# Kernel tuning notes

Measured on AMD Instinct MI355X. Metric: run time of the kernel, lower is better.

## Reference

```python
import jax, jax.numpy as jnp
import numpy as np

FG_THR = 0.7
BG_THR = 0.3
NUM_PER_IMAGE = 256
NUM_POS_MAX = int(NUM_PER_IMAGE * 0.5)  # positive_ratio = 0.5
BBOX_W = (1.0, 1.0, 1.0, 1.0)
BETA = 1.0 / 9.0


def _permute(t, C):
    # N x (A*C) x H x W -> N x (H*W*A) x C, matching RPNLoss.permute
    N, _, H, W = t.shape
    t = t.reshape(N, -1, C, H, W)
    t = jnp.transpose(t, (0, 3, 4, 1, 2))
    return t.reshape(N, -1, C)


def _iou(a, b):
    # a: [N,4], b: [M,4] -> [N,M] (with +1 box convention, as in source)
    x_tl = jnp.maximum(a[:, None, 0], b[None, :, 0])
    y_tl = jnp.maximum(a[:, None, 1], b[None, :, 1])
    x_rb = jnp.minimum(a[:, None, 2], b[None, :, 2])
    y_rb = jnp.minimum(a[:, None, 3], b[None, :, 3])
    inter = jnp.clip(x_rb - x_tl + 1.0, 0.0) * jnp.clip(y_rb - y_tl + 1.0, 0.0)
    area1 = (a[:, 2] - a[:, 0] + 1.0) * (a[:, 3] - a[:, 1] + 1.0)
    area2 = (b[:, 2] - b[:, 0] + 1.0) * (b[:, 3] - b[:, 1] + 1.0)
    return inter / (area1[:, None] + area2[None, :] - inter)


def _encode(anchors, targets):
    ws = anchors[:, 2] - anchors[:, 0] + 1.0
    hs = anchors[:, 3] - anchors[:, 1] + 1.0
    x_ctr = anchors[:, 0] + 0.5 * ws
    y_ctr = anchors[:, 1] + 0.5 * hs
    t_ws = targets[:, 2] - targets[:, 0] + 1.0
    t_hs = targets[:, 3] - targets[:, 1] + 1.0
    t_x = targets[:, 0] + 0.5 * t_ws
    t_y = targets[:, 1] + 0.5 * t_hs
    wx, wy, ww, wh = BBOX_W
    tx = wx * (t_x - x_ctr) / ws
    ty = wy * (t_y - y_ctr) / hs
    tw = ww * jnp.log(t_ws / ws)
    th = wh * jnp.log(t_hs / hs)
    return jnp.stack([tx, ty, tw, th], axis=1)


def _bce_logits(l, t):
    return jnp.maximum(l, 0.0) - l * t + jnp.log1p(jnp.exp(-jnp.abs(l)))


def _per_image(anchor, logit, breg, size, target, key):
    N = anchor.shape[0]
    ious = _iou(anchor, target)  # [N, M]
    vals = ious.max(axis=1)
    ori = jnp.argmax(ious, axis=1).astype(jnp.int32)
    inds = jnp.where(vals < BG_THR, -1, ori)
    inds = jnp.where((vals >= BG_THR) & (vals < FG_THR), -2, inds)
    # low-quality matches: anchors achieving the per-target max IoU keep their argmax
    col_max = ious.max(axis=0)
    restore = (ious == col_max[None, :]).any(axis=1)
    inds = jnp.where(restore, ori, inds)
    # filter_anchors: keep anchors fully inside the image (size = (h, w))
    inside = (anchor[:, 0] >= 0) & (anchor[:, 1] >= 0) & \
             (anchor[:, 2] <= size[1] - 1.0) & (anchor[:, 3] <= size[0] - 1.0)
    inds = jnp.where(inside, inds, -2)

    pos = inds >= 0
    neg = inds == -1
    # random sampling via random priorities + fixed-size top_k with validity masks
    r = jax.random.uniform(key, (N,))
    pos_vals, pos_idx = jax.lax.top_k(jnp.where(pos, r, -1.0), NUM_POS_MAX)
    valid_pos = pos_vals >= 0.0
    num_pos = valid_pos.sum()
    neg_vals, neg_idx = jax.lax.top_k(jnp.where(neg, r, -1.0), NUM_PER_IMAGE)
    valid_neg = (neg_vals >= 0.0) & (jnp.arange(NUM_PER_IMAGE) < (NUM_PER_IMAGE - num_pos))

    # classification loss terms (BCE with logits); pos target 1, neg target 0
    vp = valid_pos.astype(logit.dtype)
    vn = valid_neg.astype(logit.dtype)
    cls_sum = jnp.sum(_bce_logits(logit[pos_idx], 1.0) * vp) + \
              jnp.sum(_bce_logits(logit[neg_idx], 0.0) * vn)
    count = num_pos + valid_neg.sum()

    m = jnp.clip(inds[pos_idx], 0, None)
    offsets = _encode(anchor[pos_idx], target[m])
    diff = jnp.abs(breg[pos_idx] - offsets)
    sl1 = jnp.where(diff < BETA, 0.5 * diff * diff / BETA, diff - 0.5 * BETA)
    reg_sum = jnp.sum(sl1 * vp[:, None])
    return cls_sum, count, reg_sum


def reference(anchors, logits, bbox_regs, sizes, targets):
    B = anchors.shape[0]
    log = _permute(logits, 1)[..., 0]      # [B, H*W*A]
    breg = _permute(bbox_regs, 4)          # [B, H*W*A, 4]
    keys = jax.random.split(jax.random.key(42), B)
    cls_s, cnt, reg_s = jax.vmap(_per_image)(anchors, log, breg, sizes, targets, keys)
    total = jnp.sum(cnt).astype(anchors.dtype)
    cls_loss = jnp.sum(cls_s) / total
    reg_loss = jnp.sum(reg_s) / total
    return jnp.stack([cls_loss, reg_loss])


def setup_inputs() -> dict:
    key = jax.random.key(0)
    ks = jax.random.split(key, 10)
    B, A, H, W, M = 4, 3, 168, 256, 32
    N = H * W * A
    IMG_H, IMG_W = 800.0, 1333.0
    x1 = jax.random.uniform(ks[0], (B, N)) * 1200.0
    y1 = jax.random.uniform(ks[1], (B, N)) * 700.0
    aw = jax.random.uniform(ks[2], (B, N)) * 300.0 + 16.0
    ah = jax.random.uniform(ks[3], (B, N)) * 300.0 + 16.0
    anchors = jnp.stack([x1, y1, x1 + aw, y1 + ah], axis=-1)  # some out of image -> filtered
    tx1 = jax.random.uniform(ks[4], (B, M)) * 1000.0
    ty1 = jax.random.uniform(ks[5], (B, M)) * 500.0
    tw = jax.random.uniform(ks[6], (B, M)) * 250.0 + 30.0
    th = jax.random.uniform(ks[7], (B, M)) * 200.0 + 30.0
    targets = jnp.stack([tx1, ty1, jnp.minimum(tx1 + tw, IMG_W - 1.0),
                         jnp.minimum(ty1 + th, IMG_H - 1.0)], axis=-1)
    logits = jax.random.normal(ks[8], (B, A, H, W), dtype=jnp.float32)
    bbox_regs = jax.random.normal(ks[9], (B, 4 * A, H, W), dtype=jnp.float32) * 0.1
    sizes = jnp.tile(jnp.array([IMG_H, IMG_W], dtype=jnp.float32), (B, 1))
    return {"anchors": anchors, "logits": logits, "bbox_regs": bbox_regs,
            "sizes": sizes, "targets": targets}
```

## Files before the change

### kernel.cpp

```cpp
#include <hip/hip_runtime.h>
#include <stdint.h>

#define Bn 4
#define An 3
#define Hn 168
#define Wn 256
#define Mn 32
#define HWn (Hn*Wn)
#define Nn (HWn*An)
#define POS_CAP 8192
#define BND_CAP 2048
#define NPERIM 256
#define NPOSMAX 128
#define FG_THR 0.7f
#define BG_THR 0.3f
#define BETA (1.0f/9.0f)

#define OFF_KEYS   0
#define OFF_COLMAX 8
#define OFF_POSCNT 136
#define OFF_BNDCNT 140
#define OFF_BOUND  144
#define OFF_NEED   148
#define OFF_COUNT  152
#define OFF_CLS    153
#define OFF_REG    154
#define OFF_DONE   155
#define ZERO_BEG   8
#define ZERO_END   160
#define OFF_PACK   4256
#define OFF_PLIST  520352
#define OFF_BLIST  585888
#define OFF_PHIST  602272

__device__ __forceinline__ uint32_t rotl32(uint32_t v, int n) { return (v << n) | (v >> (32 - n)); }

__device__ __forceinline__ void tf2x32(uint32_t k0, uint32_t k1, uint32_t x0, uint32_t x1,
                                       uint32_t& o0, uint32_t& o1) {
    uint32_t k2 = k0 ^ k1 ^ 0x1BD11BDAu;
    x0 += k0; x1 += k1;
    x0 += x1; x1 = rotl32(x1, 13); x1 ^= x0;
    x0 += x1; x1 = rotl32(x1, 15); x1 ^= x0;
    x0 += x1; x1 = rotl32(x1, 26); x1 ^= x0;
    x0 += x1; x1 = rotl32(x1, 6);  x1 ^= x0;
    x0 += k1; x1 += k2 + 1u;
    x0 += x1; x1 = rotl32(x1, 17); x1 ^= x0;
    x0 += x1; x1 = rotl32(x1, 29); x1 ^= x0;
    x0 += x1; x1 = rotl32(x1, 16); x1 ^= x0;
    x0 += x1; x1 = rotl32(x1, 24); x1 ^= x0;
    x0 += k2; x1 += k0 + 2u;
    x0 += x1; x1 = rotl32(x1, 13); x1 ^= x0;
    x0 += x1; x1 = rotl32(x1, 15); x1 ^= x0;
    x0 += x1; x1 = rotl32(x1, 26); x1 ^= x0;
    x0 += x1; x1 = rotl32(x1, 6);  x1 ^= x0;
    x0 += k0; x1 += k1 + 3u;
    x0 += x1; x1 = rotl32(x1, 17); x1 ^= x0;
    x0 += x1; x1 = rotl32(x1, 29); x1 ^= x0;
    x0 += x1; x1 = rotl32(x1, 16); x1 ^= x0;
    x0 += x1; x1 = rotl32(x1, 24); x1 ^= x0;
    x0 += k1; x1 += k2 + 4u;
    x0 += x1; x1 = rotl32(x1, 13); x1 ^= x0;
    x0 += x1; x1 = rotl32(x1, 15); x1 ^= x0;
    x0 += x1; x1 = rotl32(x1, 26); x1 ^= x0;
    x0 += x1; x1 = rotl32(x1, 6);  x1 ^= x0;
    x0 += k2; x1 += k0 + 5u;
    o0 = x0; o1 = x1;
}

__device__ __forceinline__ uint32_t rng_m23(uint32_t k0, uint32_t k1, uint32_t i) {
    uint32_t o0, o1;
    tf2x32(k0, k1, 0u, i, o0, o1);
    return (o0 ^ o1) >> 9;
}

__device__ __forceinline__ float iou_one(float a0, float a1, float a2, float a3,
                                         float t0, float t1, float t2, float t3) {
    float xtl = fmaxf(a0, t0), ytl = fmaxf(a1, t1);
    float xrb = fminf(a2, t2), yrb = fminf(a3, t3);
    float iw = fmaxf(xrb - xtl + 1.0f, 0.0f);
    float ih = fmaxf(yrb - ytl + 1.0f, 0.0f);
    float inter = iw * ih;
    float area1 = (a2 - a0 + 1.0f) * (a3 - a1 + 1.0f);
    float area2 = (t2 - t0 + 1.0f) * (t3 - t1 + 1.0f);
    return inter * __builtin_amdgcn_rcpf(area1 + area2 - inter);
}

__global__ void k0_init(uint32_t* __restrict__ ws) {
    int t = blockIdx.x * blockDim.x + threadIdx.x;
    for (int j = ZERO_BEG + t; j < ZERO_END; j += gridDim.x * blockDim.x) ws[j] = 0u;
    if (t == 0) {
        for (int b = 0; b < Bn; ++b) {
            uint32_t o0, o1;
            tf2x32(0u, 42u, 0u, (uint32_t)b, o0, o1);
            ws[OFF_KEYS + 2*b] = o0; ws[OFF_KEYS + 2*b + 1] = o1;
        }
    }
}

#define K1_APT 4
#define K1_BLOCKS 126
#define K1_STRIDE (K1_BLOCKS * 256)
__global__ void __launch_bounds__(256) k1_colmax(const float* __restrict__ anchors,
                                                 const float* __restrict__ targets,
                                                 uint32_t* __restrict__ ws) {
    int b = blockIdx.y;
    __shared__ float part[4][Mn];
    int base = blockIdx.x * 256 + threadIdx.x;
    float4 a[K1_APT];
    #pragma unroll
    for (int k = 0; k < K1_APT; ++k)
        a[k] = ((const float4*)anchors)[b * Nn + base + k * K1_STRIDE];
    float cm[Mn];
    #pragma unroll 4
    for (int t = 0; t < Mn; ++t) {
        float4 tv = ((const float4*)targets)[b * Mn + t];
        float m0 = 0.0f;
        #pragma unroll
        for (int k = 0; k < K1_APT; ++k)
            m0 = fmaxf(m0, iou_one(a[k].x, a[k].y, a[k].z, a[k].w, tv.x, tv.y, tv.z, tv.w));
        cm[t] = m0;
    }
    #pragma unroll
    for (int t = 0; t < Mn; ++t) {
        #pragma unroll
        for (int o = 32; o > 0; o >>= 1) cm[t] = fmaxf(cm[t], __shfl_xor(cm[t], o, 64));
    }
    int wid = threadIdx.x >> 6, lane = threadIdx.x & 63;
    if (lane == 0) {
        #pragma unroll
        for (int t = 0; t < Mn; ++t) part[wid][t] = cm[t];
    }
    __syncthreads();
    if (threadIdx.x < Mn) {
        float v = fmaxf(fmaxf(part[0][threadIdx.x], part[1][threadIdx.x]),
                        fmaxf(part[2][threadIdx.x], part[3][threadIdx.x]));
        atomicMax(&ws[OFF_COLMAX + b * Mn + threadIdx.x], __float_as_uint(v));
    }
}

#define K2_APT 4
#define K2_BLOCKS 126
#define K2_STRIDE (K2_BLOCKS * 256)
__global__ void __launch_bounds__(256) k2_cat(const float* __restrict__ anchors,
                                              const float* __restrict__ targets,
                                              const float* __restrict__ sizes,
                                              uint32_t* __restrict__ ws) {
    int b = blockIdx.y;
    __shared__ uint32_t lh[1024];
    #pragma unroll
    for (int j = 0; j < 4; ++j) lh[threadIdx.x + 256 * j] = 0u;
    __syncthreads();
    int base = blockIdx.x * 256 + threadIdx.x;
    float4 av[K2_APT];
    #pragma unroll
    for (int k = 0; k < K2_APT; ++k)
        av[k] = ((const float4*)anchors)[b * Nn + base + k * K2_STRIDE];
    float rowmax[K2_APT]; int ori[K2_APT]; bool restore[K2_APT];
    #pragma unroll
    for (int k = 0; k < K2_APT; ++k) { rowmax[k] = -1.0f; ori[k] = 0; restore[k] = false; }
    #pragma unroll 4
    for (int t = 0; t < Mn; ++t) {
        float4 tv = ((const float4*)targets)[b * Mn + t];
        float cmf = __uint_as_float(ws[OFF_COLMAX + b * Mn + t]);
        #pragma unroll
        for (int k = 0; k < K2_APT; ++k) {
            float iou = iou_one(av[k].x, av[k].y, av[k].z, av[k].w, tv.x, tv.y, tv.z, tv.w);
            if (iou > rowmax[k]) { rowmax[k] = iou; ori[k] = t; }
            restore[k] = restore[k] || (iou == cmf);
        }
    }
    float sh = sizes[b * 2 + 0], sw = sizes[b * 2 + 1];
    uint32_t key0 = ws[OFF_KEYS + 2 * b], key1 = ws[OFF_KEYS + 2 * b + 1];
    #pragma unroll
    for (int k = 0; k < K2_APT; ++k) {
        int i = base + k * K2_STRIDE;
        bool inside = (av[k].x >= 0.0f) && (av[k].y >= 0.0f) &&
                      (av[k].z <= sw - 1.0f) && (av[k].w <= sh - 1.0f);
        uint32_t cat = 0;
        if (inside) {
            if (restore[k] || rowmax[k] >= FG_THR) cat = 2;
            else if (rowmax[k] < BG_THR) cat = 1;
        }
        uint32_t m = rng_m23(key0, key1, (uint32_t)i);
        ws[OFF_PACK + b * Nn + i] = m | (cat << 24);
        if (cat == 2u) {
            uint32_t p = atomicAdd(&ws[OFF_POSCNT + b], 1u);
            if (p < POS_CAP) {
                ws[OFF_PLIST + ((uint32_t)b * POS_CAP + p) * 2 + 0] = m;
                ws[OFF_PLIST + ((uint32_t)b * POS_CAP + p) * 2 + 1] = (uint32_t)i | ((uint32_t)ori[k] << 17);
            }
        } else if (cat == 1u) {
            atomicAdd(&lh[m >> 13], 1u);
        }
    }
    __syncthreads();
    uint32_t* slice = ws + OFF_PHIST + ((size_t)b * K2_BLOCKS + blockIdx.x) * 1024;
    #pragma unroll
    for (int j = 0; j < 4; ++j) {
        int idx = threadIdx.x + 256 * j;
        slice[idx] = lh[idx];
    }
}

__global__ void __launch_bounds__(256) k25_bound(uint32_t* __restrict__ ws) {
    int b = blockIdx.x;
    int t = threadIdx.x;
    __shared__ uint32_t csum[256];
    uint4 h = make_uint4(0, 0, 0, 0);
    const uint32_t* ph = ws + OFF_PHIST + (size_t)b * K2_BLOCKS * 1024;
    for (int s = 0; s < K2_BLOCKS; ++s) {
        uint4 v = ((const uint4*)(ph + (size_t)s * 1024))[t];
        h.x += v.x; h.y += v.y; h.z += v.z; h.w += v.w;
    }
    uint32_t sum = h.x + h.y + h.z + h.w;
    csum[t] = sum;
    __syncthreads();
    for (int off = 1; off < 256; off <<= 1) {
        uint32_t mine = csum[t];
        uint32_t add = (t + off < 256) ? csum[t + off] : 0u;
        __syncthreads();
        csum[t] = mine + add;
        __syncthreads();
    }
    uint32_t pc = ws[OFF_POSCNT + b];
    int num_pos = (pc < (uint32_t)NPOSMAX) ? (int)pc : NPOSMAX;
    int k_neg = NPERIM - num_pos;
    uint32_t total = csum[0];
    if ((int)total < k_neg) {
        if (t == 0) {
            ws[OFF_BOUND + b] = 0xFFFFFFFFu;
            ws[OFF_NEED + b] = 0u;
            atomicAdd(&ws[OFF_COUNT], (uint32_t)(num_pos + (int)total));
        }
        return;
    }
    uint32_t incl = csum[t];
    uint32_t next = (t < 255) ? csum[t + 1] : 0u;
    if ((int)incl >= k_neg && (int)next < k_neg) {
        int cum = (int)next;
        uint32_t hv[4] = { h.x, h.y, h.z, h.w };
        int boundary = -1, needed = 0;
        #pragma unroll
        for (int j = 3; j >= 0; --j) {
            int c = (int)hv[j];
            if (cum + c >= k_neg) { boundary = 4 * t + j; needed = k_neg - cum; break; }
            cum += c;
        }
        ws[OFF_BOUND + b] = (uint32_t)boundary;
        ws[OFF_NEED + b] = (uint32_t)needed;
        atomicAdd(&ws[OFF_COUNT], (uint32_t)(num_pos + k_neg));
    }
}

__global__ void __launch_bounds__(256) k3_neg(const float* __restrict__ logits,
                                              uint32_t* __restrict__ ws) {
    int b = blockIdx.y;
    int i = blockIdx.x * 256 + threadIdx.x;
    int bd = (int)(int32_t)ws[OFF_BOUND + b];
    uint32_t p = ws[OFF_PACK + b * Nn + i];
    uint32_t cat = p >> 24;
    float local = 0.0f;
    if (cat == 1u) {
        uint32_t m = p & 0x7FFFFFu;
        int bk = (int)(m >> 13);
        if (bk > bd) {
            int a = i % An, hw = i / An;
            float l = logits[(b * An + a) * HWn + hw];
            local = fmaxf(l, 0.0f) + log1pf(expf(-fabsf(l)));
        } else if (bk == bd) {
            uint32_t q = atomicAdd(&ws[OFF_BNDCNT + b], 1u);
            if (q < BND_CAP) {
                ws[OFF_BLIST + ((uint32_t)b * BND_CAP + q) * 2 + 0] = m;
                ws[OFF_BLIST + ((uint32_t)b * BND_CAP + q) * 2 + 1] = (uint32_t)i;
            }
        }
    }
    __shared__ float red[256];
    red[threadIdx.x] = local;
    __syncthreads();
    for (int s = 128; s > 0; s >>= 1) {
        if ((int)threadIdx.x < s) red[threadIdx.x] += red[threadIdx.x + s];
        __syncthreads();
    }
    if (threadIdx.x == 0 && red[0] != 0.0f) atomicAdd((float*)&ws[OFF_CLS], red[0]);
}

__device__ __forceinline__ bool sel_less(uint2 a, uint2 b) {
    return (a.x > b.x) || (a.x == b.x && a.y < b.y);
}

__device__ void bitonic_sort_shared(uint2* buf, int n) {
    for (int k = 2; k <= n; k <<= 1) {
        for (int j = k >> 1; j > 0; j >>= 1) {
            for (int t = (int)threadIdx.x; t < n; t += 256) {
                int ixj = t ^ j;
                if (ixj > t) {
                    uint2 x = buf[t], y = buf[ixj];
                    bool up = ((t & k) == 0);
                    bool sw = up ? sel_less(y, x) : sel_less(x, y);
                    if (sw) { buf[t] = y; buf[ixj] = x; }
                }
            }
            __syncthreads();
        }
    }
}

__global__ void __launch_bounds__(256) k4_final(const float* __restrict__ anchors,
                                                const float* __restrict__ targets,
                                                const float* __restrict__ logits,
                                                const float* __restrict__ bregs,
                                                uint32_t* __restrict__ ws,
                                                float* __restrict__ out) {
    int b = blockIdx.x;
    __shared__ uint2 buf[BND_CAP];
    __shared__ float red[256];
    float cls = 0.0f, reg = 0.0f;

    uint32_t pcu = ws[OFF_POSCNT + b];
    int pc = (pcu < (uint32_t)POS_CAP) ? (int)pcu : POS_CAP;
    const uint32_t* plist = ws + OFF_PLIST + (size_t)b * POS_CAP * 2;
    int psel = (pc < NPOSMAX) ? pc : NPOSMAX;
    bool use_buf = false;
    if (pc > NPOSMAX) {
        int n = (pc < BND_CAP) ? pc : BND_CAP;
        for (int j = (int)threadIdx.x; j < n; j += 256) buf[j] = make_uint2(plist[2*j], plist[2*j+1]);
        int npad = 1; while (npad < n) npad <<= 1;
        for (int j = (int)threadIdx.x; j < npad; j += 256) if (j >= n) buf[j] = make_uint2(0u, 0xFFFFFFFFu);
        __syncthreads();
        bitonic_sort_shared(buf, npad);
        use_buf = true;
        psel = (NPOSMAX < n) ? NPOSMAX : n;
    }
    for (int j = (int)threadIdx.x; j < psel; j += 256) {
        uint32_t packed = use_buf ? buf[j].y : plist[2*j+1];
        int i = (int)(packed & 0x1FFFFu);
        int ori = (int)(packed >> 17);
        int a = i % An, hw = i / An;
        float l = logits[(b * An + a) * HWn + hw];
        cls += fmaxf(l, 0.0f) - l + log1pf(expf(-fabsf(l)));
        float4 av = ((const float4*)anchors)[b * Nn + i];
        float4 tv = ((const float4*)targets)[b * Mn + ori];
        float aws = av.z - av.x + 1.0f, ahs = av.w - av.y + 1.0f;
        float axc = av.x + 0.5f * aws, ayc = av.y + 0.5f * ahs;
        float tws = tv.z - tv.x + 1.0f, ths = tv.w - tv.y + 1.0f;
        float txc = tv.x + 0.5f * tws, tyc = tv.y + 0.5f * ths;
        float off0 = (txc - axc) / aws;
        float off1 = (tyc - ayc) / ahs;
        float off2 = logf(tws / aws);
        float off3 = logf(ths / ahs);
        float br0 = bregs[(b * 12 + a * 4 + 0) * HWn + hw];
        float br1 = bregs[(b * 12 + a * 4 + 1) * HWn + hw];
        float br2 = bregs[(b * 12 + a * 4 + 2) * HWn + hw];
        float br3 = bregs[(b * 12 + a * 4 + 3) * HWn + hw];
        float d;
        d = fabsf(br0 - off0); reg += (d < BETA) ? 0.5f * d * d / BETA : d - 0.5f * BETA;
        d = fabsf(br1 - off1); reg += (d < BETA) ? 0.5f * d * d / BETA : d - 0.5f * BETA;
        d = fabsf(br2 - off2); reg += (d < BETA) ? 0.5f * d * d / BETA : d - 0.5f * BETA;
        d = fabsf(br3 - off3); reg += (d < BETA) ? 0.5f * d * d / BETA : d - 0.5f * BETA;
    }
    __syncthreads();

    int need = (int)ws[OFF_NEED + b];
    if (need > 0) {
        uint32_t nbu = ws[OFF_BNDCNT + b];
        int nb = (nbu < (uint32_t)BND_CAP) ? (int)nbu : BND_CAP;
        const uint32_t* blist = ws + OFF_BLIST + (size_t)b * BND_CAP * 2;
        for (int j = (int)threadIdx.x; j < nb; j += 256) buf[j] = make_uint2(blist[2*j], blist[2*j+1]);
        int npad = 1; while (npad < nb) npad <<= 1;
        for (int j = (int)threadIdx.x; j < npad; j += 256) if (j >= nb) buf[j] = make_uint2(0u, 0xFFFFFFFFu);
        __syncthreads();
        bitonic_sort_shared(buf, npad);
        int sel = (need < nb) ? need : nb;
        for (int j = (int)threadIdx.x; j < sel; j += 256) {
            int i = (int)buf[j].y;
            int a = i % An, hw = i / An;
            float l = logits[(b * An + a) * HWn + hw];
            cls += fmaxf(l, 0.0f) + log1pf(expf(-fabsf(l)));
        }
    }

    red[threadIdx.x] = cls;
    __syncthreads();
    for (int s = 128; s > 0; s >>= 1) {
        if ((int)threadIdx.x < s) red[threadIdx.x] += red[threadIdx.x + s];
        __syncthreads();
    }
    if (threadIdx.x == 0 && red[0] != 0.0f) atomicAdd((float*)&ws[OFF_CLS], red[0]);
    __syncthreads();
    red[threadIdx.x] = reg;
    __syncthreads();
    for (int s = 128; s > 0; s >>= 1) {
        if ((int)threadIdx.x < s) red[threadIdx.x] += red[threadIdx.x + s];
        __syncthreads();
    }
    if (threadIdx.x == 0) {
        if (red[0] != 0.0f) atomicAdd((float*)&ws[OFF_REG], red[0]);
        __threadfence();
        uint32_t old = atomicAdd(&ws[OFF_DONE], 1u);
        if (old == Bn - 1) {
            float cls_tot = __uint_as_float(atomicAdd(&ws[OFF_CLS], 0u));
            float reg_tot = __uint_as_float(atomicAdd(&ws[OFF_REG], 0u));
            float cnt = (float)atomicAdd(&ws[OFF_COUNT], 0u);
            out[0] = cls_tot / cnt;
            out[1] = reg_tot / cnt;
        }
    }
}

extern "C" void kernel_launch(void* const* d_in, const int* in_sizes, int n_in,
                              void* d_out, int out_size, void* d_ws, size_t ws_size,
                              hipStream_t stream) {
    const float* anchors = (const float*)d_in[0];
    const float* logits  = (const float*)d_in[1];
    const float* bregs   = (const float*)d_in[2];
    const float* sizes   = (const float*)d_in[3];
    const float* targets = (const float*)d_in[4];
    float* out = (float*)d_out;
    uint32_t* ws = (uint32_t*)d_ws;

    k0_init<<<dim3(64), dim3(256), 0, stream>>>(ws);
    k1_colmax<<<dim3(K1_BLOCKS, Bn), dim3(256), 0, stream>>>(anchors, targets, ws);
    k2_cat<<<dim3(K2_BLOCKS, Bn), dim3(256), 0, stream>>>(anchors, targets, sizes, ws);
    k25_bound<<<dim3(Bn), dim3(256), 0, stream>>>(ws);
    k3_neg<<<dim3(Nn / 256, Bn), dim3(256), 0, stream>>>(logits, ws);
    k4_final<<<dim3(Bn), dim3(256), 0, stream>>>(anchors, targets, logits, bregs, ws, out);
}
```

Baseline: 161.7 us.

## Compact negatives into a list, drop init kernel, wave-aggregate atomics

Removes the separate init kernel by having one k1 block zero the counters and derive the keys, and replaces the global atomicMax column max with per-block partials that k2 reduces itself. k2 now writes a compacted negative list using wave-level ballot atomics instead of a full packed array, and positive-list appends also use ballot-aggregated atomics. k3 then walks only the negative list with a grid-stride loop instead of scanning every anchor. This cuts one launch and much of the global traffic and contention, but k2 must first reduce the partial column maxes, and the negative list is written with no capacity bound.

```diff
diff --git a/kernel.cpp b/kernel.cpp
--- a/kernel.cpp
+++ b/kernel.cpp
@@ -10,28 +10,33 @@
 #define Nn (HWn*An)
 #define POS_CAP 8192
 #define BND_CAP 2048
+#define NEG_CAP 131072
 #define NPERIM 256
 #define NPOSMAX 128
 #define FG_THR 0.7f
 #define BG_THR 0.3f
 #define BETA (1.0f/9.0f)
 
-#define OFF_KEYS   0
-#define OFF_COLMAX 8
-#define OFF_POSCNT 136
-#define OFF_BNDCNT 140
-#define OFF_BOUND  144
-#define OFF_NEED   148
-#define OFF_COUNT  152
-#define OFF_CLS    153
-#define OFF_REG    154
-#define OFF_DONE   155
-#define ZERO_BEG   8
-#define ZERO_END   160
-#define OFF_PACK   4256
-#define OFF_PLIST  520352
-#define OFF_BLIST  585888
-#define OFF_PHIST  602272
+#define NBLK 126
+#define APT 4
+#define STRIDE (NBLK * 256)
+
+#define OFF_POSCNT 0
+#define OFF_NEGCNT 4
+#define OFF_BNDCNT 8
+#define OFF_BOUND  12
+#define OFF_NEED   16
+#define OFF_COUNT  20
+#define OFF_CLS    21
+#define OFF_REG    22
+#define OFF_DONE   23
+#define OFF_KEYS   24
+#define OFF_PCM    32
+#define OFF_PHIST  16160
+#define OFF_FHIST  532256
+#define OFF_PLIST  536352
+#define OFF_BLIST  601888
+#define OFF_NLIST  618272
 
 __device__ __forceinline__ uint32_t rotl32(uint32_t v, int n) { return (v << n) | (v >> (32 - n)); }
 
@@ -85,38 +90,33 @@
     return inter * __builtin_amdgcn_rcpf(area1 + area2 - inter);
 }
 
-__global__ void k0_init(uint32_t* __restrict__ ws) {
-    int t = blockIdx.x * blockDim.x + threadIdx.x;
-    for (int j = ZERO_BEG + t; j < ZERO_END; j += gridDim.x * blockDim.x) ws[j] = 0u;
-    if (t == 0) {
-        for (int b = 0; b < Bn; ++b) {
-            uint32_t o0, o1;
-            tf2x32(0u, 42u, 0u, (uint32_t)b, o0, o1);
-            ws[OFF_KEYS + 2*b] = o0; ws[OFF_KEYS + 2*b + 1] = o1;
-        }
-    }
-}
-
-#define K1_APT 4
-#define K1_BLOCKS 126
-#define K1_STRIDE (K1_BLOCKS * 256)
 __global__ void __launch_bounds__(256) k1_colmax(const float* __restrict__ anchors,
                                                  const float* __restrict__ targets,
                                                  uint32_t* __restrict__ ws) {
-    int b = blockIdx.y;
+    int b = blockIdx.y, j = blockIdx.x, tid = threadIdx.x;
+    if (b == 0 && j == 0) {
+        if (tid < 24) ws[tid] = 0u;
+        if (tid == 0) {
+            for (int bb = 0; bb < Bn; ++bb) {
+                uint32_t o0, o1;
+                tf2x32(0u, 42u, 0u, (uint32_t)bb, o0, o1);
+                ws[OFF_KEYS + 2*bb] = o0; ws[OFF_KEYS + 2*bb + 1] = o1;
+            }
+        }
+    }
     __shared__ float part[4][Mn];
-    int base = blockIdx.x * 256 + threadIdx.x;
-    float4 a[K1_APT];
-    #pragma unroll
-    for (int k = 0; k < K1_APT; ++k)
-        a[k] = ((const float4*)anchors)[b * Nn + base + k * K1_STRIDE];
+    int base = j * 256 + tid;
+    float4 a[APT];
+    #pragma unroll
+    for (int k = 0; k < APT; ++k)
+        a[k] = ((const float4*)anchors)[b * Nn + base + k * STRIDE];
     float cm[Mn];
     #pragma unroll 4
     for (int t = 0; t < Mn; ++t) {
         float4 tv = ((const float4*)targets)[b * Mn + t];
         float m0 = 0.0f;
         #pragma unroll
-        for (int k = 0; k < K1_APT; ++k)
+        for (int k = 0; k < APT; ++k)
             m0 = fmaxf(m0, iou_one(a[k].x, a[k].y, a[k].z, a[k].w, tv.x, tv.y, tv.z, tv.w));
         cm[t] = m0;
     }
@@ -125,55 +125,70 @@
         #pragma unroll
         for (int o = 32; o > 0; o >>= 1) cm[t] = fmaxf(cm[t], __shfl_xor(cm[t], o, 64));
     }
-    int wid = threadIdx.x >> 6, lane = threadIdx.x & 63;
+    int wid = tid >> 6, lane = tid & 63;
     if (lane == 0) {
         #pragma unroll
         for (int t = 0; t < Mn; ++t) part[wid][t] = cm[t];
     }
     __syncthreads();
-    if (threadIdx.x < Mn) {
-        float v = fmaxf(fmaxf(part[0][threadIdx.x], part[1][threadIdx.x]),
-                        fmaxf(part[2][threadIdx.x], part[3][threadIdx.x]));
-        atomicMax(&ws[OFF_COLMAX + b * Mn + threadIdx.x], __float_as_uint(v));
-    }
-}
-
-#define K2_APT 4
-#define K2_BLOCKS 126
-#define K2_STRIDE (K2_BLOCKS * 256)
+    if (tid < Mn) {
+        float v = fmaxf(fmaxf(part[0][tid], part[1][tid]),
+                        fmaxf(part[2][tid], part[3][tid]));
+        ws[OFF_PCM + ((size_t)b * NBLK + j) * Mn + tid] = __float_as_uint(v);
+    }
+}
+
 __global__ void __launch_bounds__(256) k2_cat(const float* __restrict__ anchors,
                                               const float* __restrict__ targets,
                                               const float* __restrict__ sizes,
                                               uint32_t* __restrict__ ws) {
-    int b = blockIdx.y;
+    int b = blockIdx.y, j = blockIdx.x, tid = threadIdx.x;
+    __shared__ float cmf[Mn];
+    __shared__ float redf[256];
     __shared__ uint32_t lh[1024];
-    #pragma unroll
-    for (int j = 0; j < 4; ++j) lh[threadIdx.x + 256 * j] = 0u;
-    __syncthreads();
-    int base = blockIdx.x * 256 + threadIdx.x;
-    float4 av[K2_APT];
-    #pragma unroll
-    for (int k = 0; k < K2_APT; ++k)
-        av[k] = ((const float4*)anchors)[b * Nn + base + k * K2_STRIDE];
-    float rowmax[K2_APT]; int ori[K2_APT]; bool restore[K2_APT];
-    #pragma unroll
-    for (int k = 0; k < K2_APT; ++k) { rowmax[k] = -1.0f; ori[k] = 0; restore[k] = false; }
+    {
+        int t = tid & 31, sub = tid >> 5;
+        float acc = 0.0f;
+        for (int jj = sub; jj < NBLK; jj += 8)
+            acc = fmaxf(acc, __uint_as_float(ws[OFF_PCM + ((size_t)b * NBLK + jj) * Mn + t]));
+        redf[tid] = acc;
+        __syncthreads();
+        if (sub == 0) {
+            #pragma unroll
+            for (int q = 1; q < 8; ++q) acc = fmaxf(acc, redf[t + 32 * q]);
+            cmf[t] = acc;
+        }
+    }
+    #pragma unroll
+    for (int q = 0; q < 4; ++q) lh[tid + 256 * q] = 0u;
+    __syncthreads();
+
+    int base = j * 256 + tid;
+    float4 av[APT];
+    #pragma unroll
+    for (int k = 0; k < APT; ++k)
+        av[k] = ((const float4*)anchors)[b * Nn + base + k * STRIDE];
+    float rowmax[APT]; int ori[APT]; bool restore[APT];
+    #pragma unroll
+    for (int k = 0; k < APT; ++k) { rowmax[k] = -1.0f; ori[k] = 0; restore[k] = false; }
     #pragma unroll 4
     for (int t = 0; t < Mn; ++t) {
         float4 tv = ((const float4*)targets)[b * Mn + t];
-        float cmf = __uint_as_float(ws[OFF_COLMAX + b * Mn + t]);
+        float cmv = cmf[t];
         #pragma unroll
-        for (int k = 0; k < K2_APT; ++k) {
+        for (int k = 0; k < APT; ++k) {
             float iou = iou_one(av[k].x, av[k].y, av[k].z, av[k].w, tv.x, tv.y, tv.z, tv.w);
             if (iou > rowmax[k]) { rowmax[k] = iou; ori[k] = t; }
-            restore[k] = restore[k] || (iou == cmf);
+            restore[k] = restore[k] || (iou == cmv);
         }
     }
     float sh = sizes[b * 2 + 0], sw = sizes[b * 2 + 1];
     uint32_t key0 = ws[OFF_KEYS + 2 * b], key1 = ws[OFF_KEYS + 2 * b + 1];
-    #pragma unroll
-    for (int k = 0; k < K2_APT; ++k) {
-        int i = base + k * K2_STRIDE;
+    int lane = tid & 63;
+    unsigned long long lt_mask = (lane == 63) ? 0x7FFFFFFFFFFFFFFFull : ((1ull << lane) - 1ull);
+    #pragma unroll
+    for (int k = 0; k < APT; ++k) {
+        int i = base + k * STRIDE;
         bool inside = (av[k].x >= 0.0f) && (av[k].y >= 0.0f) &&
                       (av[k].z <= sw - 1.0f) && (av[k].w <= sh - 1.0f);
         uint32_t cat = 0;
@@ -182,33 +197,44 @@
             else if (rowmax[k] < BG_THR) cat = 1;
         }
         uint32_t m = rng_m23(key0, key1, (uint32_t)i);
-        ws[OFF_PACK + b * Nn + i] = m | (cat << 24);
-        if (cat == 2u) {
-            uint32_t p = atomicAdd(&ws[OFF_POSCNT + b], 1u);
-            if (p < POS_CAP) {
-                ws[OFF_PLIST + ((uint32_t)b * POS_CAP + p) * 2 + 0] = m;
-                ws[OFF_PLIST + ((uint32_t)b * POS_CAP + p) * 2 + 1] = (uint32_t)i | ((uint32_t)ori[k] << 17);
+        unsigned long long pmask = __ballot(cat == 2u);
+        if (pmask) {
+            int leader = __ffsll((long long)pmask) - 1;
+            uint32_t bb = 0;
+            if (lane == leader) bb = atomicAdd(&ws[OFF_POSCNT + b], (uint32_t)__popcll(pmask));
+            bb = __shfl(bb, leader, 64);
+            if (cat == 2u) {
+                uint32_t p = bb + (uint32_t)__popcll(pmask & lt_mask);
+                if (p < POS_CAP)
+                    ((uint2*)(ws + OFF_PLIST))[(size_t)b * POS_CAP + p] =
+                        make_uint2(m, (uint32_t)i | ((uint32_t)ori[k] << 17));
             }
-        } else if (cat == 1u) {
-            atomicAdd(&lh[m >> 13], 1u);
-        }
-    }
-    __syncthreads();
-    uint32_t* slice = ws + OFF_PHIST + ((size_t)b * K2_BLOCKS + blockIdx.x) * 1024;
-    #pragma unroll
-    for (int j = 0; j < 4; ++j) {
-        int idx = threadIdx.x + 256 * j;
-        slice[idx] = lh[idx];
-    }
+        }
+        unsigned long long nmask = __ballot(cat == 1u);
+        if (nmask) {
+            int leader = __ffsll((long long)nmask) - 1;
+            uint32_t bb = 0;
+            if (lane == leader) bb = atomicAdd(&ws[OFF_NEGCNT + b], (uint32_t)__popcll(nmask));
+            bb = __shfl(bb, leader, 64);
+            if (cat == 1u) {
+                uint32_t p = bb + (uint32_t)__popcll(nmask & lt_mask);
+                ((uint2*)(ws + OFF_NLIST))[(size_t)b * NEG_CAP + p] = make_uint2(m, (uint32_t)i);
+                atomicAdd(&lh[m >> 13], 1u);
+            }
+        }
+    }
+    __syncthreads();
+    uint32_t* slice = ws + OFF_PHIST + ((size_t)b * NBLK + j) * 1024;
+    #pragma unroll
+    for (int q = 0; q < 4; ++q) slice[tid + 256 * q] = lh[tid + 256 * q];
 }
 
 __global__ void __launch_bounds__(256) k25_bound(uint32_t* __restrict__ ws) {
-    int b = blockIdx.x;
-    int t = threadIdx.x;
+    int b = blockIdx.x, t = threadIdx.x;
     __shared__ uint32_t csum[256];
     uint4 h = make_uint4(0, 0, 0, 0);
-    const uint32_t* ph = ws + OFF_PHIST + (size_t)b * K2_BLOCKS * 1024;
-    for (int s = 0; s < K2_BLOCKS; ++s) {
+    const uint32_t* ph = ws + OFF_PHIST + (size_t)b * NBLK * 1024;
+    for (int s = 0; s < NBLK; ++s) {
         uint4 v = ((const uint4*)(ph + (size_t)s * 1024))[t];
         h.x += v.x; h.y += v.y; h.z += v.z; h.w += v.w;
     }
@@ -241,9 +267,9 @@
         uint32_t hv[4] = { h.x, h.y, h.z, h.w };
         int boundary = -1, needed = 0;
         #pragma unroll
-        for (int j = 3; j >= 0; --j) {
-            int c = (int)hv[j];
-            if (cum + c >= k_neg) { boundary = 4 * t + j; needed = k_neg - cum; break; }
+        for (int q = 3; q >= 0; --q) {
+            int c = (int)hv[q];
+            if (cum + c >= k_neg) { boundary = 4 * t + q; needed = k_neg - cum; break; }
             cum += c;
         }
         ws[OFF_BOUND + b] = (uint32_t)boundary;
@@ -255,24 +281,22 @@
 __global__ void __launch_bounds__(256) k3_neg(const float* __restrict__ logits,
                                               uint32_t* __restrict__ ws) {
     int b = blockIdx.y;
-    int i = blockIdx.x * 256 + threadIdx.x;
     int bd = (int)(int32_t)ws[OFF_BOUND + b];
-    uint32_t p = ws[OFF_PACK + b * Nn + i];
-    uint32_t cat = p >> 24;
+    int cnt = (int)ws[OFF_NEGCNT + b];
+    const uint2* nlist = (const uint2*)(ws + OFF_NLIST) + (size_t)b * NEG_CAP;
     float local = 0.0f;
-    if (cat == 1u) {
-        uint32_t m = p & 0x7FFFFFu;
-        int bk = (int)(m >> 13);
+    for (int idx = blockIdx.x * 256 + (int)threadIdx.x; idx < cnt; idx += NBLK * 256) {
+        uint2 e = nlist[idx];
+        int bk = (int)(e.x >> 13);
         if (bk > bd) {
+            int i = (int)e.y;
             int a = i % An, hw = i / An;
             float l = logits[(b * An + a) * HWn + hw];
-            local = fmaxf(l, 0.0f) + log1pf(expf(-fabsf(l)));
+            local += fmaxf(l, 0.0f) + log1pf(expf(-fabsf(l)));
         } else if (bk == bd) {
             uint32_t q = atomicAdd(&ws[OFF_BNDCNT + b], 1u);
-            if (q < BND_CAP) {
-                ws[OFF_BLIST + ((uint32_t)b * BND_CAP + q) * 2 + 0] = m;
-                ws[OFF_BLIST + ((uint32_t)b * BND_CAP + q) * 2 + 1] = (uint32_t)i;
-            }
+            if (q < BND_CAP)
+                ((uint2*)(ws + OFF_BLIST))[(size_t)b * BND_CAP + q] = e;
         }
     }
     __shared__ float red[256];
@@ -312,28 +336,28 @@
                                                 const float* __restrict__ bregs,
                                                 uint32_t* __restrict__ ws,
                                                 float* __restrict__ out) {
-    int b = blockIdx.x;
+    int b = blockIdx.x, tid = threadIdx.x;
     __shared__ uint2 buf[BND_CAP];
     __shared__ float red[256];
     float cls = 0.0f, reg = 0.0f;
 
     uint32_t pcu = ws[OFF_POSCNT + b];
     int pc = (pcu < (uint32_t)POS_CAP) ? (int)pcu : POS_CAP;
-    const uint32_t* plist = ws + OFF_PLIST + (size_t)b * POS_CAP * 2;
+    const uint2* plist = (const uint2*)(ws + OFF_PLIST) + (size_t)b * POS_CAP;
     int psel = (pc < NPOSMAX) ? pc : NPOSMAX;
     bool use_buf = false;
     if (pc > NPOSMAX) {
         int n = (pc < BND_CAP) ? pc : BND_CAP;
-        for (int j = (int)threadIdx.x; j < n; j += 256) buf[j] = make_uint2(plist[2*j], plist[2*j+1]);
+        for (int t = tid; t < n; t += 256) buf[t] = plist[t];
         int npad = 1; while (npad < n) npad <<= 1;
-        for (int j = (int)threadIdx.x; j < npad; j += 256) if (j >= n) buf[j] = make_uint2(0u, 0xFFFFFFFFu);
+        for (int t = tid; t < npad; t += 256) if (t >= n) buf[t] = make_uint2(0u, 0xFFFFFFFFu);
         __syncthreads();
         bitonic_sort_shared(buf, npad);
         use_buf = true;
         psel = (NPOSMAX < n) ? NPOSMAX : n;
     }
-    for (int j = (int)threadIdx.x; j < psel; j += 256) {
-        uint32_t packed = use_buf ? buf[j].y : plist[2*j+1];
+    for (int t = tid; t < psel; t += 256) {
+        uint32_t packed = use_buf ? buf[t].y : plist[t].y;
         int i = (int)(packed & 0x1FFFFu);
         int ori = (int)(packed >> 17);
         int a = i % An, hw = i / An;
@@ -365,36 +389,36 @@
     if (need > 0) {
         uint32_t nbu = ws[OFF_BNDCNT + b];
         int nb = (nbu < (uint32_t)BND_CAP) ? (int)nbu : BND_CAP;
-        const uint32_t* blist = ws + OFF_BLIST + (size_t)b * BND_CAP * 2;
-        for (int j = (int)threadIdx.x; j < nb; j += 256) buf[j] = make_uint2(blist[2*j], blist[2*j+1]);
+        const uint2* blist = (const uint2*)(ws + OFF_BLIST) + (size_t)b * BND_CAP;
+        for (int t = tid; t < nb; t += 256) buf[t] = blist[t];
         int npad = 1; while (npad < nb) npad <<= 1;
-        for (int j = (int)threadIdx.x; j < npad; j += 256) if (j >= nb) buf[j] = make_uint2(0u, 0xFFFFFFFFu);
+        for (int t = tid; t < npad; t += 256) if (t >= nb) buf[t] = make_uint2(0u, 0xFFFFFFFFu);
         __syncthreads();
         bitonic_sort_shared(buf, npad);
         int sel = (need < nb) ? need : nb;
-        for (int j = (int)threadIdx.x; j < sel; j += 256) {
-            int i = (int)buf[j].y;
+        for (int t = tid; t < sel; t += 256) {
+            int i = (int)buf[t].y;
             int a = i % An, hw = i / An;
             float l = logits[(b * An + a) * HWn + hw];
             cls += fmaxf(l, 0.0f) + log1pf(expf(-fabsf(l)));
         }
     }
 
-    red[threadIdx.x] = cls;
+    red[tid] = cls;
     __syncthreads();
     for (int s = 128; s > 0; s >>= 1) {
-        if ((int)threadIdx.x < s) red[threadIdx.x] += red[threadIdx.x + s];
-        __syncthreads();
-    }
-    if (threadIdx.x == 0 && red[0] != 0.0f) atomicAdd((float*)&ws[OFF_CLS], red[0]);
-    __syncthreads();
-    red[threadIdx.x] = reg;
+        if (tid < s) red[tid] += red[tid + s];
+        __syncthreads();
+    }
+    if (tid == 0 && red[0] != 0.0f) atomicAdd((float*)&ws[OFF_CLS], red[0]);
+    __syncthreads();
+    red[tid] = reg;
     __syncthreads();
     for (int s = 128; s > 0; s >>= 1) {
-        if ((int)threadIdx.x < s) red[threadIdx.x] += red[threadIdx.x + s];
-        __syncthreads();
-    }
-    if (threadIdx.x == 0) {
+        if (tid < s) red[tid] += red[tid + s];
+        __syncthreads();
+    }
+    if (tid == 0) {
         if (red[0] != 0.0f) atomicAdd((float*)&ws[OFF_REG], red[0]);
         __threadfence();
         uint32_t old = atomicAdd(&ws[OFF_DONE], 1u);
@@ -419,10 +443,9 @@
     float* out = (float*)d_out;
     uint32_t* ws = (uint32_t*)d_ws;
 
-    k0_init<<<dim3(64), dim3(256), 0, stream>>>(ws);
-    k1_colmax<<<dim3(K1_BLOCKS, Bn), dim3(256), 0, stream>>>(anchors, targets, ws);
-    k2_cat<<<dim3(K2_BLOCKS, Bn), dim3(256), 0, stream>>>(anchors, targets, sizes, ws);
+    k1_colmax<<<dim3(NBLK, Bn), dim3(256), 0, stream>>>(anchors, targets, ws);
+    k2_cat<<<dim3(NBLK, Bn), dim3(256), 0, stream>>>(anchors, targets, sizes, ws);
     k25_bound<<<dim3(Bn), dim3(256), 0, stream>>>(ws);
-    k3_neg<<<dim3(Nn / 256, Bn), dim3(256), 0, stream>>>(logits, ws);
+    k3_neg<<<dim3(NBLK, Bn), dim3(256), 0, stream>>>(logits, ws);
     k4_final<<<dim3(Bn), dim3(256), 0, stream>>>(anchors, targets, logits, bregs, ws, out);
 }
```

New measurement: 248.7 us. 53.8% more time.
